# Kernel tuning notes

Measured on AMD Instinct MI355X. Metric: run time of the kernel, lower is better.

The kernel has to match this reference:

```python
import jax, jax.numpy as jnp
import numpy as np

B, S, HID = 4, 4096, 1024
H, D = 16, 64  # num_head, attn_dim
EPS = 1e-6


def setup_inputs() -> dict:
    key = jax.random.key(0)
    ks = jax.random.split(key, 9)
    sc = 1.0 / np.sqrt(HID)
    return {
        "x": jax.random.normal(ks[0], (B, S, HID), jnp.float32),
        "Wq": jax.random.normal(ks[1], (HID, H * D), jnp.float32) * sc,
        "bq": jnp.zeros((H * D,), jnp.float32),
        "Wk": jax.random.normal(ks[2], (HID, H * D), jnp.float32) * sc,
        "bk": jnp.zeros((H * D,), jnp.float32),
        "Wv": jax.random.normal(ks[3], (HID, H * D), jnp.float32) * sc,
        "bv": jnp.zeros((H * D,), jnp.float32),
        "Wo": jax.random.normal(ks[4], (H * D, HID), jnp.float32) * sc,
        "bo": jnp.zeros((HID,), jnp.float32),
    }


def _phi(x):
    # feature_map == 'elu': elu(x) + 1
    return jax.nn.elu(x) + 1.0


def reference(x, Wq, bq, Wk, bk, Wv, bv, Wo, bo):
    bs, n, _ = x.shape
    # projections -> [b, n, h, d], then scan axis first -> [n, b, h, d]
    Q = _phi((x @ Wq + bq).reshape(bs, n, H, D)).transpose(1, 0, 2, 3)
    K = _phi((x @ Wk + bk).reshape(bs, n, H, D)).transpose(1, 0, 2, 3)
    V = (x @ Wv + bv).reshape(bs, n, H, D).transpose(1, 0, 2, 3)

    KV0 = jnp.zeros((bs, H, D, D), x.dtype)
    Ks0 = jnp.zeros((bs, H, D), x.dtype)

    def step(carry, qkv):
        KV, Ks = carry
        qi, ki, vi = qkv  # each [b, h, d]
        KV = KV + jnp.einsum('bhd,bhe->bhde', ki, vi)
        Ks = Ks + ki
        num = jnp.einsum('bhd,bhde->bhe', qi, KV)
        den = jnp.einsum('bhd,bhd->bh', qi, Ks)
        return (KV, Ks), num / (den[..., None] + EPS)

    _, out = jax.lax.scan(step, (KV0, Ks0), (Q, K, V))  # out: [n, b, h, d]
    out = out.transpose(1, 0, 2, 3).reshape(bs, n, H * D)
    return out @ Wo + bo
```

## Files before the change

### kernel.cpp

```cpp
#include <hip/hip_runtime.h>
#include <stdint.h>


#define DEVI __device__ __forceinline__

typedef __attribute__((ext_vector_type(8))) short bf16x8;
typedef __attribute__((ext_vector_type(4))) float f32x4;
typedef unsigned short u16;

DEVI u16 f2bf(float f) {
  union { float f; uint32_t u; } x; x.f = f;
  return (u16)((x.u + 0x7FFFu + ((x.u >> 16) & 1u)) >> 16);
}
DEVI float bf2f(u16 u) {
  union { uint32_t u; float f; } x; x.u = ((uint32_t)u) << 16;
  return x.f;
}
DEVI f32x4 mfma16(bf16x8 a, bf16x8 b, f32x4 c) {
  return __builtin_amdgcn_mfma_f32_16x16x32_bf16(a, b, c, 0, 0, 0);
}

typedef __attribute__((address_space(3))) void* lds_vp;
typedef const __attribute__((address_space(1))) void* glb_vp;
DEVI void gload_lds16(const void* g, void* l) {
  __builtin_amdgcn_global_load_lds((glb_vp)g, (lds_vp)l, 16, 0, 0);
}

static constexpr int Ss  = 4096;
static constexpr int Hh  = 16;
static constexpr int CC  = 64;
static constexpr int NCC = Ss / CC;

__global__ __launch_bounds__(256) void cvt_bf16_k(const float* __restrict__ in,
                                                  u16* __restrict__ out, int n8) {
  const int i = blockIdx.x * 256 + threadIdx.x;
  if (i >= n8) return;
  const float4* p = (const float4*)(in + (size_t)i * 8);
  const float4 a = p[0], b = p[1];
  union { uint4 v; u16 s[8]; } u;
  u.s[0] = f2bf(a.x); u.s[1] = f2bf(a.y); u.s[2] = f2bf(a.z); u.s[3] = f2bf(a.w);
  u.s[4] = f2bf(b.x); u.s[5] = f2bf(b.y); u.s[6] = f2bf(b.z); u.s[7] = f2bf(b.w);
  ((uint4*)out)[i] = u.v;
}

__global__ __launch_bounds__(256) void transpose_cvt_k(const float* __restrict__ in,
                                                       u16* __restrict__ out) {
  __shared__ float tl[32][33];
  const int tx = threadIdx.x & 31, ty = threadIdx.x >> 5;
  const int bx = blockIdx.x, by = blockIdx.y;
#pragma unroll
  for (int j = 0; j < 4; ++j)
    tl[ty + j * 8][tx] = in[(size_t)(by * 32 + ty + j * 8) * 1024 + bx * 32 + tx];
  __syncthreads();
#pragma unroll
  for (int j = 0; j < 4; ++j)
    out[(size_t)(bx * 32 + ty + j * 8) * 1024 + by * 32 + tx] = f2bf(tl[tx][ty + j * 8]);
}

template <bool FUSED, bool OUTF32>
__global__ __launch_bounds__(512, 2) void gemm256_k(const u16* __restrict__ A,
                                                    const u16* __restrict__ BT,
                                                    const float* __restrict__ b0,
                                                    const float* __restrict__ b1,
                                                    const float* __restrict__ b2,
                                                    void* __restrict__ out,
                                                    int M, int K) {
  __shared__ __attribute__((aligned(16))) u16 lds[65536];
  const int t = threadIdx.x, lane = t & 63, w = t >> 6;
  const int wm = w >> 2, wn = w & 3;

  const int nx = gridDim.x;
  const int nwg = nx * gridDim.y;
  const int bid = blockIdx.y * nx + blockIdx.x;
  const int swz = (bid & 7) * (nwg >> 3) + (bid >> 3);
  const int bx = swz % nx, by = swz / nx;
  const int m0 = by * 256, n0 = bx * 256;

  const u16* gA = A + (size_t)m0 * K;
  const u16* gB = BT + (size_t)n0 * K;

  const int sr = t >> 2;
  const int sc = (t & 3) ^ ((sr >> 1) & 3);
  auto stage = [&](const u16* gm, u16* dst, int kof) {
    gload_lds16(gm + (size_t)sr * K + kof + sc * 8, dst + t * 8);
    gload_lds16(gm + (size_t)(sr + 128) * K + kof + sc * 8, dst + 4096 + t * 8);
  };

  f32x4 acc[8][4];
#pragma unroll
  for (int i = 0; i < 8; ++i)
#pragma unroll
    for (int j = 0; j < 4; ++j) acc[i][j] = f32x4{0.f, 0.f, 0.f, 0.f};

  stage(gA, lds, 0);          stage(gB, lds + 32768, 0);
  stage(gA, lds + 8192, 32);  stage(gB, lds + 40960, 32);

  const int fr = lane & 15, kq = lane >> 4;
  const int rdko = ((kq ^ ((fr >> 1) & 3)) << 3);
  const int arow0 = wm * 128 + fr;
  const int brow0 = wn * 64 + fr;

  const int nk = K >> 6;
  for (int kt = 0; kt < nk; ++kt) {
    const int buf = kt & 1;
    u16* Ax = lds + buf * 16384;
    u16* Bx = lds + 32768 + buf * 16384;
    u16* Ay = lds + (buf ^ 1) * 16384;
    u16* By = lds + 32768 + (buf ^ 1) * 16384;
    const bool pf = (kt + 1 < nk);
    const int kon = (kt + 1) << 6;
    bf16x8 af[8], bg0, bg1;

#pragma unroll
    for (int half = 0; half < 2; ++half) {
      u16* Axh = Ax + half * 8192;
      u16* Bxh = Bx + half * 8192;
      if (half == 0 || pf) asm volatile("s_waitcnt vmcnt(4)" ::: "memory");
      else                 asm volatile("s_waitcnt vmcnt(0)" ::: "memory");
      __builtin_amdgcn_s_barrier();
      if (pf) stage(gA, Ay + half * 8192, kon + half * 32);
#pragma unroll
      for (int fi = 0; fi < 8; ++fi)
        af[fi] = *(const bf16x8*)(Axh + (arow0 + fi * 16) * 32 + rdko);
      bg0 = *(const bf16x8*)(Bxh + brow0 * 32 + rdko);
      bg1 = *(const bf16x8*)(Bxh + (brow0 + 16) * 32 + rdko);
      asm volatile("s_waitcnt lgkmcnt(0)" ::: "memory");
      __builtin_amdgcn_sched_barrier(0);
      __builtin_amdgcn_s_setprio(1);
#pragma unroll
      for (int fi = 0; fi < 8; ++fi) {
        acc[fi][0] = mfma16(af[fi], bg0, acc[fi][0]);
        acc[fi][1] = mfma16(af[fi], bg1, acc[fi][1]);
      }
      __builtin_amdgcn_s_setprio(0);
      __builtin_amdgcn_sched_barrier(0);
      if (pf) stage(gB, By + half * 8192, kon + half * 32);
      bg0 = *(const bf16x8*)(Bxh + (brow0 + 32) * 32 + rdko);
      bg1 = *(const bf16x8*)(Bxh + (brow0 + 48) * 32 + rdko);
      asm volatile("s_waitcnt lgkmcnt(0)" ::: "memory");
      __builtin_amdgcn_sched_barrier(0);
      __builtin_amdgcn_s_setprio(1);
#pragma unroll
      for (int fi = 0; fi < 8; ++fi) {
        acc[fi][2] = mfma16(af[fi], bg0, acc[fi][2]);
        acc[fi][3] = mfma16(af[fi], bg1, acc[fi][3]);
      }
      __builtin_amdgcn_s_setprio(0);
      __builtin_amdgcn_sched_barrier(0);
    }
  }

  const int rowg = (lane >> 4) * 4;
  if constexpr (!OUTF32) {
    __syncthreads();
    const int seg  = FUSED ? (n0 >> 10) : 0;
    const int lcol0 = FUSED ? (n0 & 1023) : n0;
    const float* bp = b0;
    if constexpr (FUSED) bp = (seg == 0) ? b0 : (seg == 1) ? b1 : b2;
#pragma unroll
    for (int fj = 0; fj < 4; ++fj) {
      const int col = wn * 64 + fj * 16 + fr;
      const float bv = bp[lcol0 + col];
#pragma unroll
      for (int fi = 0; fi < 8; ++fi) {
#pragma unroll
        for (int rr = 0; rr < 4; ++rr) {
          const int row = wm * 128 + fi * 16 + rowg + rr;
          float v = acc[fi][fj][rr] + bv;
          if (FUSED && seg < 2) v = (v > 0.f) ? (v + 1.f) : __expf(v);
          lds[row * 256 + (((col >> 3) ^ ((row >> 2) & 31)) << 3) + (col & 7)] = f2bf(v);
        }
      }
    }
    __syncthreads();
    u16* outp = (u16*)out + (size_t)seg * M * 1024 + (size_t)m0 * 1024 + lcol0;
#pragma unroll
    for (int it = 0; it < 16; ++it) {
      const int g = it * 512 + t;
      const int row = g >> 5, c16 = g & 31;
      const uint4 v = *(const uint4*)&lds[row * 256 + ((c16 ^ ((row >> 2) & 31)) << 3)];
      *(uint4*)(outp + (size_t)row * 1024 + c16 * 8) = v;
    }
  } else {
    float* flds = (float*)lds;
#pragma unroll
    for (int pass = 0; pass < 2; ++pass) {
      __syncthreads();
      if (wm == pass) {
#pragma unroll
        for (int fj = 0; fj < 4; ++fj) {
          const int col = wn * 64 + fj * 16 + fr;
          const float bv = b0[n0 + col];
#pragma unroll
          for (int fi = 0; fi < 8; ++fi) {
#pragma unroll
            for (int rr = 0; rr < 4; ++rr) {
              const int rl = fi * 16 + rowg + rr;
              flds[rl * 256 + (((col >> 2) ^ ((rl >> 2) & 63)) << 2) + (col & 3)] =
                  acc[fi][fj][rr] + bv;
            }
          }
        }
      }
      __syncthreads();
      float* outp = (float*)out + (size_t)(m0 + pass * 128) * 1024 + n0;
#pragma unroll
      for (int it = 0; it < 16; ++it) {
        const int g = it * 512 + t;
        const int row = g >> 6, c16 = g & 63;
        const uint4 v = *(const uint4*)&flds[row * 256 + ((c16 ^ ((row >> 2) & 63)) << 2)];
        *(uint4*)(outp + (size_t)row * 1024 + c16 * 4) = v;
      }
    }
  }
}

__global__ __launch_bounds__(256) void chunk_kv_k(const u16* __restrict__ Kb,
                                                  const u16* __restrict__ Vb,
                                                  u16* __restrict__ KVTc,
                                                  float* __restrict__ Ksc) {
  const int c = blockIdx.x, h = blockIdx.y, b = blockIdx.z;
  __shared__ u16 KT[64][72], VT[64][72];
  const int t = threadIdx.x, lane = t & 63, w = t >> 6;
  {
    const int i = t >> 2, c0 = (t & 3) * 16;
    const size_t g = ((size_t)(b * Ss + c * CC + i)) * 1024 + h * 64 + c0;
    const u16* kp = Kb + g;
    const u16* vp = Vb + g;
#pragma unroll
    for (int j = 0; j < 16; ++j) { KT[c0 + j][i] = kp[j]; VT[c0 + j][i] = vp[j]; }
  }
  __syncthreads();
  f32x4 acc[4];
#pragma unroll
  for (int j = 0; j < 4; ++j) acc[j] = f32x4{0.f, 0.f, 0.f, 0.f};
  const int fr = lane & 15, kq = (lane >> 4) * 8;
#pragma unroll
  for (int kk = 0; kk < 2; ++kk) {
    const bf16x8 av = *(const bf16x8*)&VT[w * 16 + fr][kk * 32 + kq];
#pragma unroll
    for (int fj = 0; fj < 4; ++fj) {
      const bf16x8 bk = *(const bf16x8*)&KT[fj * 16 + fr][kk * 32 + kq];
      acc[fj] = mfma16(av, bk, acc[fj]);
    }
  }
  const size_t base = ((size_t)((b * Hh + h) * NCC + c)) * 4096;
#pragma unroll
  for (int fj = 0; fj < 4; ++fj)
#pragma unroll
    for (int rr = 0; rr < 4; ++rr) {
      const int e = w * 16 + (lane >> 4) * 4 + rr;
      const int d = fj * 16 + fr;
      KVTc[base + (size_t)e * 64 + d] = f2bf(acc[fj][rr]);
    }
  if (t < 64) {
    float s = 0.f;
#pragma unroll
    for (int ii = 0; ii < 8; ++ii) {
      const bf16x8 kv = *(const bf16x8*)&KT[t][ii * 8];
#pragma unroll
      for (int j = 0; j < 8; ++j) s += bf2f((u16)kv[j]);
    }
    Ksc[((size_t)((b * Hh + h) * NCC + c)) * 64 + t] = s;
  }
}

__global__ __launch_bounds__(256) void prefix_k(const u16* __restrict__ KVTc,
                                                const float* __restrict__ Ksc,
                                                u16* __restrict__ KVpreT,
                                                float* __restrict__ Kspre) {
  const int bh = blockIdx.x, eg = blockIdx.y;
  const int t = threadIdx.x;
  const int e4 = eg * 1024 + t * 4;
  const u16* src = KVTc + (size_t)bh * NCC * 4096 + e4;
  u16* dst = KVpreT + (size_t)bh * NCC * 4096 + e4;
  const float* kss = Ksc + (size_t)bh * NCC * 64 + t;
  float* ksd = Kspre + (size_t)bh * NCC * 64 + t;
  float run[4] = {0.f, 0.f, 0.f, 0.f};
  float rk = 0.f;
  for (int c = 0; c < NCC; ++c) {
    union { uint2 v; u16 s[4]; } in, ov;
    in.v = *(const uint2*)(src + (size_t)c * 4096);
#pragma unroll
    for (int j = 0; j < 4; ++j) { ov.s[j] = f2bf(run[j]); run[j] += bf2f(in.s[j]); }
    *(uint2*)(dst + (size_t)c * 4096) = ov.v;
    if (eg == 0 && t < 64) { ksd[(size_t)c * 64] = rk; rk += kss[(size_t)c * 64]; }
  }
}

__global__ __launch_bounds__(256) void chunk_out_k(const u16* __restrict__ Qb,
                                                   const u16* __restrict__ Kb,
                                                   const u16* __restrict__ Vb,
                                                   const u16* __restrict__ KVpreT,
                                                   const float* __restrict__ Kspre,
                                                   u16* __restrict__ attn) {
  const int c = blockIdx.x, h = blockIdx.y, b = blockIdx.z;
  const int bh = b * Hh + h;
  __shared__ u16 Ql[64][72], Kl[64][72], VT[64][72], Pl[64][72];
  __shared__ float den[64];
  const int t = threadIdx.x, lane = t & 63, w = t >> 6;

  {
    const int i = t >> 2, c0 = (t & 3) * 16;
    const size_t g = ((size_t)(b * Ss + c * CC + i)) * 1024 + h * 64 + c0;
    const uint4* qp = (const uint4*)(Qb + g);
    uint4* qd = (uint4*)&Ql[i][c0]; qd[0] = qp[0]; qd[1] = qp[1];
    const uint4* kp = (const uint4*)(Kb + g);
    uint4* kd = (uint4*)&Kl[i][c0]; kd[0] = kp[0]; kd[1] = kp[1];
    const u16* vp = Vb + g;
#pragma unroll
    for (int j = 0; j < 16; ++j) VT[c0 + j][i] = vp[j];
  }
  __syncthreads();

  f32x4 sacc[4];
#pragma unroll
  for (int fj = 0; fj < 4; ++fj) sacc[fj] = f32x4{0.f, 0.f, 0.f, 0.f};
#pragma unroll
  for (int kd = 0; kd < 2; ++kd) {
    const bf16x8 aq = *(const bf16x8*)&Ql[w * 16 + (lane & 15)][kd * 32 + (lane >> 4) * 8];
#pragma unroll
    for (int fj = 0; fj < 4; ++fj) {
      const bf16x8 bk = *(const bf16x8*)&Kl[fj * 16 + (lane & 15)][kd * 32 + (lane >> 4) * 8];
      sacc[fj] = mfma16(aq, bk, sacc[fj]);
    }
  }
  float rowsum[4] = {0.f, 0.f, 0.f, 0.f};
#pragma unroll
  for (int fj = 0; fj < 4; ++fj) {
#pragma unroll
    for (int rr = 0; rr < 4; ++rr) {
      const int i_loc = w * 16 + (lane >> 4) * 4 + rr;
      const int j_loc = fj * 16 + (lane & 15);
      const float v = (j_loc <= i_loc) ? sacc[fj][rr] : 0.f;
      Pl[i_loc][j_loc] = f2bf(v);
      rowsum[rr] += v;
    }
  }
#pragma unroll
  for (int off = 1; off < 16; off <<= 1) {
#pragma unroll
    for (int rr = 0; rr < 4; ++rr) rowsum[rr] += __shfl_xor(rowsum[rr], off, 64);
  }
  if ((lane & 15) == 0) {
#pragma unroll
    for (int rr = 0; rr < 4; ++rr) den[w * 16 + (lane >> 4) * 4 + rr] = rowsum[rr];
  }
  __syncthreads();
  {
    const int i = t >> 2, part = t & 3;
    const float* ksp = Kspre + ((size_t)(bh * NCC + c)) * 64 + part * 16;
    float s = 0.f;
#pragma unroll
    for (int sg = 0; sg < 2; ++sg) {
      const bf16x8 q = *(const bf16x8*)&Ql[i][part * 16 + sg * 8];
#pragma unroll
      for (int j = 0; j < 8; ++j) s += bf2f((u16)q[j]) * ksp[sg * 8 + j];
    }
    s += __shfl_xor(s, 1, 64);
    s += __shfl_xor(s, 2, 64);
    if (part == 0) den[i] = den[i] + s + 1e-6f;
  }
  __syncthreads();

  f32x4 oacc[4];
#pragma unroll
  for (int fj = 0; fj < 4; ++fj) oacc[fj] = f32x4{0.f, 0.f, 0.f, 0.f};
  const u16* kvb = KVpreT + ((size_t)(bh * NCC + c)) * 4096;
#pragma unroll
  for (int ks2 = 0; ks2 < 2; ++ks2) {
    const bf16x8 aq = *(const bf16x8*)&Ql[w * 16 + (lane & 15)][ks2 * 32 + (lane >> 4) * 8];
#pragma unroll
    for (int fj = 0; fj < 4; ++fj) {
      const bf16x8 bv =
          *(const bf16x8*)(kvb + (size_t)(fj * 16 + (lane & 15)) * 64 + ks2 * 32 + (lane >> 4) * 8);
      oacc[fj] = mfma16(aq, bv, oacc[fj]);
    }
  }
#pragma unroll
  for (int ks3 = 0; ks3 < 2; ++ks3) {
    const bf16x8 ap = *(const bf16x8*)&Pl[w * 16 + (lane & 15)][ks3 * 32 + (lane >> 4) * 8];
#pragma unroll
    for (int fj = 0; fj < 4; ++fj) {
      const bf16x8 bv = *(const bf16x8*)&VT[fj * 16 + (lane & 15)][ks3 * 32 + (lane >> 4) * 8];
      oacc[fj] = mfma16(ap, bv, oacc[fj]);
    }
  }
#pragma unroll
  for (int fj = 0; fj < 4; ++fj) {
#pragma unroll
    for (int rr = 0; rr < 4; ++rr) {
      const int i_loc = w * 16 + (lane >> 4) * 4 + rr;
      const int e = fj * 16 + (lane & 15);
      const float v = oacc[fj][rr] / den[i_loc];
      attn[((size_t)(b * Ss + c * CC + i_loc)) * 1024 + h * 64 + e] = f2bf(v);
    }
  }
}

extern "C" void kernel_launch(void* const* d_in, const int* in_sizes, int n_in,
                              void* d_out, int out_size, void* d_ws, size_t ws_size,
                              hipStream_t stream) {
  (void)in_sizes; (void)n_in; (void)out_size; (void)ws_size;
  const float* x  = (const float*)d_in[0];
  const float* Wq = (const float*)d_in[1];
  const float* bq = (const float*)d_in[2];
  const float* Wk = (const float*)d_in[3];
  const float* bk = (const float*)d_in[4];
  const float* Wv = (const float*)d_in[5];
  const float* bv = (const float*)d_in[6];
  const float* Wo = (const float*)d_in[7];
  const float* bo = (const float*)d_in[8];
  float* out = (float*)d_out;
  char* ws = (char*)d_ws;

  size_t off = 0;
  auto take = [&](size_t bytes) { size_t r = off; off += (bytes + 255) & ~(size_t)255; return r; };
  const size_t WQKV_B = (size_t)3072 * 1024 * 2;
  const size_t WT_B   = (size_t)1024 * 1024 * 2;
  const size_t BIG_B  = (size_t)16384 * 1024 * 2;
  const size_t KVT_B  = (size_t)64 * NCC * 4096 * 2;
  const size_t KS_B   = (size_t)64 * NCC * 64 * 4;

  u16* WqkvT  = (u16*)(ws + take(WQKV_B));
  u16* WoT    = (u16*)(ws + take(WT_B));
  size_t shared_off = take(BIG_B);
  u16* xbf    = (u16*)(ws + shared_off);
  u16* KVTc   = (u16*)(ws + shared_off);
  u16* attn   = (u16*)(ws + shared_off);
  u16* Qb     = (u16*)(ws + take(BIG_B));
  u16* Kb     = (u16*)(ws + take(BIG_B));
  u16* Vb     = (u16*)(ws + take(BIG_B));
  u16* KVpreT = (u16*)(ws + take(KVT_B));
  float* Ksc  = (float*)(ws + take(KS_B));
  float* Kspre= (float*)(ws + take(KS_B));

  const dim3 blk(256);
  cvt_bf16_k<<<dim3(8192), blk, 0, stream>>>(x, xbf, 16384 * 1024 / 8);
  const dim3 gT(32, 32);
  transpose_cvt_k<<<gT, blk, 0, stream>>>(Wq, WqkvT);
  transpose_cvt_k<<<gT, blk, 0, stream>>>(Wk, WqkvT + (size_t)1024 * 1024);
  transpose_cvt_k<<<gT, blk, 0, stream>>>(Wv, WqkvT + (size_t)2048 * 1024);
  transpose_cvt_k<<<gT, blk, 0, stream>>>(Wo, WoT);

  gemm256_k<true, false><<<dim3(12, 64), dim3(512), 0, stream>>>(
      xbf, WqkvT, bq, bk, bv, Qb, 16384, 1024);

  const dim3 gC(NCC, Hh, 4);
  chunk_kv_k<<<gC, blk, 0, stream>>>(Kb, Vb, KVTc, Ksc);
  prefix_k<<<dim3(64, 4), blk, 0, stream>>>(KVTc, Ksc, KVpreT, Kspre);
  chunk_out_k<<<gC, blk, 0, stream>>>(Qb, Kb, Vb, KVpreT, Kspre, attn);

  gemm256_k<false, true><<<dim3(4, 64), dim3(512), 0, stream>>>(
      attn, WoT, bo, NULL, NULL, out, 16384, 1024);
}
```

Measured before the change: 267.4 us.

## Merge prep kernels, stage chunk outputs through LDS, prefetch prefix scan

After: 264.9 us. Within noise of the previous version (-0.9%).

```diff
diff --git a/kernel.cpp b/kernel.cpp
--- a/kernel.cpp
+++ b/kernel.cpp
@@ -31,23 +31,32 @@
 static constexpr int CC  = 64;
 static constexpr int NCC = Ss / CC;
 
-__global__ __launch_bounds__(256) void cvt_bf16_k(const float* __restrict__ in,
-                                                  u16* __restrict__ out, int n8) {
-  const int i = blockIdx.x * 256 + threadIdx.x;
-  if (i >= n8) return;
-  const float4* p = (const float4*)(in + (size_t)i * 8);
-  const float4 a = p[0], b = p[1];
-  union { uint4 v; u16 s[8]; } u;
-  u.s[0] = f2bf(a.x); u.s[1] = f2bf(a.y); u.s[2] = f2bf(a.z); u.s[3] = f2bf(a.w);
-  u.s[4] = f2bf(b.x); u.s[5] = f2bf(b.y); u.s[6] = f2bf(b.z); u.s[7] = f2bf(b.w);
-  ((uint4*)out)[i] = u.v;
-}
-
-__global__ __launch_bounds__(256) void transpose_cvt_k(const float* __restrict__ in,
-                                                       u16* __restrict__ out) {
+__global__ __launch_bounds__(256) void prep_k(const float* __restrict__ x,
+                                              const float* __restrict__ w0,
+                                              const float* __restrict__ w1,
+                                              const float* __restrict__ w2,
+                                              const float* __restrict__ w3,
+                                              u16* __restrict__ xbf,
+                                              u16* __restrict__ dqkv,
+                                              u16* __restrict__ dwo) {
   __shared__ float tl[32][33];
+  const int bid = blockIdx.x;
+  if (bid < 8192) {
+    const int i = bid * 256 + threadIdx.x;
+    const float4* p = (const float4*)(x + (size_t)i * 8);
+    const float4 a = p[0], b = p[1];
+    union { uint4 v; u16 s[8]; } u;
+    u.s[0] = f2bf(a.x); u.s[1] = f2bf(a.y); u.s[2] = f2bf(a.z); u.s[3] = f2bf(a.w);
+    u.s[4] = f2bf(b.x); u.s[5] = f2bf(b.y); u.s[6] = f2bf(b.z); u.s[7] = f2bf(b.w);
+    ((uint4*)xbf)[i] = u.v;
+    return;
+  }
+  const int wz = bid - 8192;
+  const int z = wz >> 10, wl = wz & 1023;
+  const int bx = wl & 31, by = wl >> 5;
+  const float* in = (z == 0) ? w0 : (z == 1) ? w1 : (z == 2) ? w2 : w3;
+  u16* out = (z < 3) ? (dqkv + (size_t)z * 1024 * 1024) : dwo;
   const int tx = threadIdx.x & 31, ty = threadIdx.x >> 5;
-  const int bx = blockIdx.x, by = blockIdx.y;
 #pragma unroll
   for (int j = 0; j < 4; ++j)
     tl[ty + j * 8][tx] = in[(size_t)(by * 32 + ty + j * 8) * 1024 + bx * 32 + tx];
@@ -209,7 +218,7 @@
         const int g = it * 512 + t;
         const int row = g >> 6, c16 = g & 63;
         const uint4 v = *(const uint4*)&flds[row * 256 + ((c16 ^ ((row >> 2) & 63)) << 2)];
-        *(uint4*)(outp + (size_t)row * 1024 + c16 * 4) = v;
+        *(uint4*)(outp + (size_t)row * 1024 + n0 * 0 + c16 * 4) = v;
       }
     }
   }
@@ -244,25 +253,29 @@
       acc[fj] = mfma16(av, bk, acc[fj]);
     }
   }
-  const size_t base = ((size_t)((b * Hh + h) * NCC + c)) * 4096;
-#pragma unroll
-  for (int fj = 0; fj < 4; ++fj)
-#pragma unroll
-    for (int rr = 0; rr < 4; ++rr) {
-      const int e = w * 16 + (lane >> 4) * 4 + rr;
-      const int d = fj * 16 + fr;
-      KVTc[base + (size_t)e * 64 + d] = f2bf(acc[fj][rr]);
-    }
+  float ksv = 0.f;
   if (t < 64) {
-    float s = 0.f;
 #pragma unroll
     for (int ii = 0; ii < 8; ++ii) {
       const bf16x8 kv = *(const bf16x8*)&KT[t][ii * 8];
 #pragma unroll
-      for (int j = 0; j < 8; ++j) s += bf2f((u16)kv[j]);
-    }
-    Ksc[((size_t)((b * Hh + h) * NCC + c)) * 64 + t] = s;
-  }
+      for (int j = 0; j < 8; ++j) ksv += bf2f((u16)kv[j]);
+    }
+  }
+  __syncthreads();
+#pragma unroll
+  for (int fj = 0; fj < 4; ++fj)
+#pragma unroll
+    for (int rr = 0; rr < 4; ++rr)
+      VT[w * 16 + (lane >> 4) * 4 + rr][fj * 16 + fr] = f2bf(acc[fj][rr]);
+  __syncthreads();
+  const size_t base = ((size_t)((b * Hh + h) * NCC + c)) * 4096;
+  {
+    const int row = t >> 2, q8 = (t & 3) * 8;
+    *(uint4*)(KVTc + base + (size_t)row * 64 + q8)      = *(const uint4*)&VT[row][q8];
+    *(uint4*)(KVTc + base + (size_t)row * 64 + q8 + 32) = *(const uint4*)&VT[row][q8 + 32];
+  }
+  if (t < 64) Ksc[((size_t)((b * Hh + h) * NCC + c)) * 64 + t] = ksv;
 }
 
 __global__ __launch_bounds__(256) void prefix_k(const u16* __restrict__ KVTc,
@@ -276,15 +289,33 @@
   u16* dst = KVpreT + (size_t)bh * NCC * 4096 + e4;
   const float* kss = Ksc + (size_t)bh * NCC * 64 + t;
   float* ksd = Kspre + (size_t)bh * NCC * 64 + t;
+  const bool dok = (eg == 0 && t < 64);
+
+  uint2 buf[8];
+  float kbuf[8];
+#pragma unroll
+  for (int j = 0; j < 8; ++j) {
+    buf[j] = *(const uint2*)(src + (size_t)j * 4096);
+    kbuf[j] = dok ? kss[(size_t)j * 64] : 0.f;
+  }
   float run[4] = {0.f, 0.f, 0.f, 0.f};
   float rk = 0.f;
-  for (int c = 0; c < NCC; ++c) {
-    union { uint2 v; u16 s[4]; } in, ov;
-    in.v = *(const uint2*)(src + (size_t)c * 4096);
-#pragma unroll
-    for (int j = 0; j < 4; ++j) { ov.s[j] = f2bf(run[j]); run[j] += bf2f(in.s[j]); }
-    *(uint2*)(dst + (size_t)c * 4096) = ov.v;
-    if (eg == 0 && t < 64) { ksd[(size_t)c * 64] = rk; rk += kss[(size_t)c * 64]; }
+  for (int g = 0; g < 8; ++g) {
+#pragma unroll
+    for (int j = 0; j < 8; ++j) {
+      const int c = g * 8 + j;
+      union { uint2 v; u16 s[4]; } in, ov;
+      in.v = buf[j];
+      const float kin = kbuf[j];
+      if (c + 8 < NCC) {
+        buf[j] = *(const uint2*)(src + (size_t)(c + 8) * 4096);
+        if (dok) kbuf[j] = kss[(size_t)(c + 8) * 64];
+      }
+#pragma unroll
+      for (int k = 0; k < 4; ++k) { ov.s[k] = f2bf(run[k]); run[k] += bf2f(in.s[k]); }
+      *(uint2*)(dst + (size_t)c * 4096) = ov.v;
+      if (dok) { ksd[(size_t)c * 64] = rk; rk += kin; }
+    }
   }
 }
 
@@ -386,15 +417,21 @@
       oacc[fj] = mfma16(ap, bv, oacc[fj]);
     }
   }
+  __syncthreads();
 #pragma unroll
   for (int fj = 0; fj < 4; ++fj) {
 #pragma unroll
     for (int rr = 0; rr < 4; ++rr) {
       const int i_loc = w * 16 + (lane >> 4) * 4 + rr;
-      const int e = fj * 16 + (lane & 15);
-      const float v = oacc[fj][rr] / den[i_loc];
-      attn[((size_t)(b * Ss + c * CC + i_loc)) * 1024 + h * 64 + e] = f2bf(v);
-    }
+      Pl[i_loc][fj * 16 + (lane & 15)] = f2bf(oacc[fj][rr] / den[i_loc]);
+    }
+  }
+  __syncthreads();
+  {
+    const int row = t >> 2, q8 = (t & 3) * 8;
+    u16* ap2 = attn + ((size_t)(b * Ss + c * CC + row)) * 1024 + h * 64;
+    *(uint4*)(ap2 + q8)      = *(const uint4*)&Pl[row][q8];
+    *(uint4*)(ap2 + q8 + 32) = *(const uint4*)&Pl[row][q8 + 32];
   }
 }
 
@@ -436,12 +473,7 @@
   float* Kspre= (float*)(ws + take(KS_B));
 
   const dim3 blk(256);
-  cvt_bf16_k<<<dim3(8192), blk, 0, stream>>>(x, xbf, 16384 * 1024 / 8);
-  const dim3 gT(32, 32);
-  transpose_cvt_k<<<gT, blk, 0, stream>>>(Wq, WqkvT);
-  transpose_cvt_k<<<gT, blk, 0, stream>>>(Wk, WqkvT + (size_t)1024 * 1024);
-  transpose_cvt_k<<<gT, blk, 0, stream>>>(Wv, WqkvT + (size_t)2048 * 1024);
-  transpose_cvt_k<<<gT, blk, 0, stream>>>(Wo, WoT);
+  prep_k<<<dim3(12288), blk, 0, stream>>>(x, Wq, Wk, Wv, Wo, xbf, WqkvT, WoT);
 
   gemm256_k<true, false><<<dim3(12, 64), dim3(512), 0, stream>>>(
       xbf, WqkvT, bq, bk, bv, Qb, 16384, 1024);
```
